# Kernel tuning notes

Hardware: AMD Instinct MI355X
Metric: run time of the kernel (lower is better)

The kernel has to match this reference:

```python
import jax, jax.numpy as jnp
import numpy as np


def setup_inputs() -> dict:
    key = jax.random.key(0)
    k_x, k_idx, k_sgn = jax.random.split(key, 3)
    batch, original_dim, proj_dim, c = 32, 1000000, 4096, 8
    x = jax.random.normal(k_x, (batch, original_dim), dtype=jnp.float32)
    rand_indices = jax.random.randint(k_idx, (original_dim, c), 0, proj_dim, dtype=jnp.int32)
    # random signs in {-1, +1}, matching torch.randint(0,2)*2-1 cast to int8
    rand_signs = (jax.random.randint(k_sgn, (original_dim, c), 0, 2, dtype=jnp.int32) * 2 - 1)
    return {"x": x, "rand_indices": rand_indices, "rand_signs": rand_signs,
            "proj_dim": proj_dim, "c": c}


def reference(x, rand_indices, rand_signs, proj_dim, c):
    # SJLT: each input coordinate d is scattered to c random output buckets
    # with random sign; normalized by 1/sqrt(c) so the sketch preserves norms.
    scale = jnp.asarray(1.0 / np.sqrt(c), dtype=x.dtype)
    batch = x.shape[0]
    out = jnp.zeros((batch, proj_dim), dtype=x.dtype)
    # c is a small fixed constant; loop over it, vectorize over batch & features.
    for j in range(c):
        vals = x * rand_signs[:, j].astype(x.dtype)      # [B, D]
        out = out.at[:, rand_indices[:, j]].add(vals)     # scatter-add along proj dim
    return out * scale
```

## Files before the change

### kernel.cpp

```cpp
#include <hip/hip_runtime.h>
#include <hip/hip_fp16.h>


#define D_TOTAL 1000000
#define PROJ    4096
#define C_SK    8
#define NE      (D_TOTAL * C_SK)
#define SCALE   0.35355339059327373f

#define NSEG    16
#define SEG_D   62500
#define CAPA2   8448
#define BINCAP_A 96
#define CAPH    96
#define TILE    4096
#define NBLK_A  ((NE + TILE - 1) / TILE)
#define NBLK_T  ((D_TOTAL + 255) / 256)
#define NSLICE  (NSEG * 2)

#define SMEM_FUSED 25088

#define CURA_OFF   0
#define XT_OFF     16384
#define XT_SZ      ((size_t)D_TOTAL * 32 * 2)
#define LISTA_OFF  (XT_OFF + XT_SZ)
#define LISTA_SZ   ((size_t)NSEG * 64 * CAPA2 * 4)
#define PART_OFF   (LISTA_OFF + LISTA_SZ)
#define PART_SZ    ((size_t)NSLICE * PROJ * 32 * 4)
#define WS_NEED    (PART_OFF + PART_SZ)

__global__ void init_cursors_kernel(int* __restrict__ curA) {
    int i = blockIdx.x * blockDim.x + threadIdx.x;
    if (i < NSEG * 64) curA[i] = i * CAPA2;
}

template<int BC>
__device__ __forceinline__ void rank_and_stage(bool ok, int kb, int payload,
                                               int* __restrict__ cnt,
                                               int* __restrict__ stage,
                                               int* __restrict__ gcur,
                                               int* __restrict__ glist,
                                               int gcur_idx, int glim) {
    if (ok) {
        const int pos = atomicAdd(&cnt[kb], 1);
        if (pos < BC) {
            stage[kb * BC + pos] = payload;
        } else {
            const int gp = atomicAdd(&gcur[gcur_idx], 1);
            if (gp < glim) glist[gp] = payload;
        }
    }
}

template<int BC>
__device__ __forceinline__ void flush_bins(int* __restrict__ cnt,
                                           int* __restrict__ basek,
                                           const int* __restrict__ stage,
                                           int* __restrict__ gcur,
                                           int* __restrict__ glist,
                                           int gidx0, int capPer) {
    const int tid = threadIdx.x;
    if (tid < 64) {
        const int m = min(cnt[tid], BC);
        cnt[tid]   = m;
        basek[tid] = atomicAdd(&gcur[gidx0 + tid], m);
    }
    __syncthreads();
    const int w = tid >> 6, lane = tid & 63;
    #pragma unroll 1
    for (int bi = 0; bi < 16; ++bi) {
        const int kb  = w * 16 + bi;
        const int m   = cnt[kb];
        const int gb  = basek[kb];
        const int lim = (gidx0 + kb + 1) * capPer;
        for (int i = lane; i < m; i += 64)
            if (gb + i < lim) glist[gb + i] = stage[kb * BC + i];
    }
}

__device__ __forceinline__ void pass_a_body(int abid, char* smem,
                                            const int* __restrict__ idx,
                                            const int* __restrict__ sgn,
                                            int* __restrict__ curA,
                                            int* __restrict__ listA) {
    int* stage = (int*)smem;
    int* cnt   = (int*)(smem + 64 * BINCAP_A * 4);
    int* basek = cnt + 64;
    const int tid = threadIdx.x;
    if (tid < 64) cnt[tid] = 0;
    __syncthreads();

    const int d_lo = abid * 512;
    const int seg  = d_lo / SEG_D;
    const bool boundary = ((d_lo + 511) / SEG_D) != seg;
    const int v0 = abid * (TILE / 4);

    #pragma unroll 1
    for (int k = 0; k < TILE / 1024; ++k) {
        const int vi = v0 + k * 256 + tid;
        const bool okv = vi < NE / 4;
        int4 i4 = {0,0,0,0}, s4 = {0,0,0,0};
        if (okv) { i4 = ((const int4*)idx)[vi]; s4 = ((const int4*)sgn)[vi]; }
        const int g0 = vi * 4;
        #pragma unroll
        for (int m = 0; m < 4; ++m) {
            const int bucket = (m == 0) ? i4.x : (m == 1) ? i4.y : (m == 2) ? i4.z : i4.w;
            const int sg     = (m == 0) ? s4.x : (m == 1) ? s4.y : (m == 2) ? s4.z : s4.w;
            const int kb = okv ? (bucket >> 6) : 0;
            const int payload = (g0 + m) | ((bucket & 63) << 24)
                              | (int)((unsigned)sg & 0x80000000u);
            if (!boundary) {
                rank_and_stage<BINCAP_A>(okv, kb, payload, cnt, stage, curA, listA,
                                         seg * 64 + kb, (seg * 64 + kb + 1) * CAPA2);
            } else if (okv) {
                const int segE = ((g0 + m) >> 3) / SEG_D;
                const int bin  = segE * 64 + kb;
                const int gp = atomicAdd(&curA[bin], 1);
                if (gp < (bin + 1) * CAPA2) listA[gp] = payload;
            }
        }
    }
    __syncthreads();
    flush_bins<BINCAP_A>(cnt, basek, stage, curA, listA, seg * 64, CAPA2);
}

__device__ __forceinline__ void transpose_body(int tbid, char* smem,
                                               const float* __restrict__ x,
                                               unsigned short* __restrict__ xT) {
    unsigned short (*tile)[260] = (unsigned short(*)[260])smem;
    const int tid = threadIdx.x;
    const int d0  = tbid * 256;
    const int row = tid >> 3;
    const int c8  = tid & 7;

    if (d0 + 256 <= D_TOTAL) {
        #pragma unroll
        for (int k = 0; k < 8; ++k) {
            const int c = (c8 + 8 * k) * 4;
            const float4 v = *(const float4*)(x + (size_t)row * D_TOTAL + d0 + c);
            unsigned short h[4];
            h[0] = __half_as_ushort(__float2half(v.x));
            h[1] = __half_as_ushort(__float2half(v.y));
            h[2] = __half_as_ushort(__float2half(v.z));
            h[3] = __half_as_ushort(__float2half(v.w));
            *(uint2*)&tile[row][c] = *(const uint2*)h;
        }
    } else {
        for (int k = 0; k < 8; ++k) {
            const int c = (c8 + 8 * k) * 4;
            for (int m = 0; m < 4; ++m) {
                const int d = d0 + c + m;
                tile[row][c + m] = __half_as_ushort(
                    __float2half((d < D_TOTAL) ? x[(size_t)row * D_TOTAL + d] : 0.f));
            }
        }
    }
    __syncthreads();

    const int part = tid & 3;
    #pragma unroll
    for (int k = 0; k < 4; ++k) {
        const int dl = k * 64 + (tid >> 2);
        if (d0 + dl < D_TOTAL) {
            unsigned short h[8];
            #pragma unroll
            for (int i = 0; i < 8; ++i)
                h[i] = tile[part * 8 + i][dl];
            *(uint4*)(xT + ((size_t)(d0 + dl)) * 32 + part * 8) = *(const uint4*)h;
        }
    }
}

__global__ __launch_bounds__(256, 6)
void pass_a_transpose_kernel(const int* __restrict__ idx, const int* __restrict__ sgn,
                             int* __restrict__ curA, int* __restrict__ listA,
                             const float* __restrict__ x, unsigned short* __restrict__ xT) {
    __shared__ char smem[SMEM_FUSED];
    const int id = blockIdx.x;
    if ((id % 3 == 0) && (id / 3 < NBLK_A)) {
        pass_a_body(id / 3, smem, idx, sgn, curA, listA);
    } else {
        const int tbid = id - id / 3 - ((id % 3) ? 1 : 0);
        if (tbid < NBLK_T) transpose_body(tbid, smem, x, xT);
    }
}

__global__ __launch_bounds__(256, 6)
void gather_part_kernel(const int* __restrict__ curA, const int* __restrict__ listA,
                        const unsigned short* __restrict__ xT,
                        float* __restrict__ partial, float* __restrict__ out) {
    __shared__ int stage[64 * CAPH];
    __shared__ int cnt[64];
    const int tid = threadIdx.x;
    const int gid = blockIdx.x;
    const int seg  = (gid & 7) + 8 * (gid >> 10);
    const int rest = (gid >> 3) & 127;
    const int kbA  = rest >> 1;
    const int half = rest & 1;
    const int part = seg * 64 + kbA;

    if (tid < 64) cnt[tid] = 0;
    __syncthreads();

    const int pstart = part * CAPA2;
    const int pcount = min(curA[part] - pstart, CAPA2);
    const int hn = (pcount + 1) >> 1;
    const int t0 = half * hn;
    const int t1 = min(t0 + hn, pcount);

    for (int i = t0 + tid; i < t1; i += 256) {
        const int e  = listA[pstart + i];
        const int kb = (e >> 24) & 63;
        const int pos = atomicAdd(&cnt[kb], 1);
        if (pos < CAPH) {
            stage[kb * CAPH + pos] = e;
        } else {
            int d = (e & 0x7FFFFF) >> 3;
            d = min(d, D_TOTAL - 1);
            const float s = (e < 0) ? -SCALE : SCALE;
            const int p = kbA * 64 + kb;
            for (int b = 0; b < 32; ++b) {
                const float v = __half2float(*(const __half*)(xT + (size_t)d * 32 + b));
                unsafeAtomicAdd(out + (size_t)b * PROJ + p, s * v);
            }
        }
    }
    __syncthreads();

    const int w    = tid >> 6;
    const int lane = tid & 63;
    const int slot = lane >> 2;
    const int bq   = lane & 3;
    #pragma unroll 1
    for (int bi = 0; bi < 16; ++bi) {
        const int kb = w * 16 + bi;
        const int n  = min(cnt[kb], CAPH);
        float a0=0.f,a1=0.f,a2=0.f,a3=0.f,a4=0.f,a5=0.f,a6=0.f,a7=0.f;
        #pragma unroll 2
        for (int base = 0; base < n; base += 16) {
            const int  e  = base + slot;
            const bool ok = e < n;
            const int  pl = stage[kb * CAPH + (ok ? e : 0)];
            int d = (pl & 0x7FFFFF) >> 3;
            d = min(d, D_TOTAL - 1);
            const float s = ok ? ((pl < 0) ? -1.f : 1.f) : 0.f;
            const uint4 hv = *(const uint4*)(xT + (size_t)d * 32 + bq * 8);
            float2 f;
            f = __half22float2(*(const __half2*)&hv.x); a0 = fmaf(s, f.x, a0); a1 = fmaf(s, f.y, a1);
            f = __half22float2(*(const __half2*)&hv.y); a2 = fmaf(s, f.x, a2); a3 = fmaf(s, f.y, a3);
            f = __half22float2(*(const __half2*)&hv.z); a4 = fmaf(s, f.x, a4); a5 = fmaf(s, f.y, a5);
            f = __half22float2(*(const __half2*)&hv.w); a6 = fmaf(s, f.x, a6); a7 = fmaf(s, f.y, a7);
        }
        #pragma unroll
        for (int m = 4; m <= 32; m <<= 1) {
            a0 += __shfl_xor(a0, m, 64); a1 += __shfl_xor(a1, m, 64);
            a2 += __shfl_xor(a2, m, 64); a3 += __shfl_xor(a3, m, 64);
            a4 += __shfl_xor(a4, m, 64); a5 += __shfl_xor(a5, m, 64);
            a6 += __shfl_xor(a6, m, 64); a7 += __shfl_xor(a7, m, 64);
        }
        if (lane < 4) {
            float v[8] = {a0,a1,a2,a3,a4,a5,a6,a7};
            const size_t slice = (size_t)(seg * 2 + half);
            float* dst = partial + (slice * PROJ + (size_t)(kbA * 64 + kb)) * 32 + lane * 8;
            #pragma unroll
            for (int i = 0; i < 8; ++i) dst[i] = v[i];
        }
    }
}

__global__ __launch_bounds__(256)
void reduce_kernel(const float* __restrict__ partial, float* __restrict__ out) {
    const int gtid = blockIdx.x * 256 + threadIdx.x;
    const int p = gtid & (PROJ - 1);
    const int b = gtid >> 12;
    float s = 0.f;
    #pragma unroll
    for (int sg = 0; sg < NSLICE; ++sg)
        s += partial[((size_t)(sg * PROJ + p)) * 32 + b];
    const size_t o = (size_t)b * PROJ + p;
    out[o] = out[o] + s * SCALE;
}

#define BG 8
#define NCHUNK 64
#define BLOCK 1024
__global__ __launch_bounds__(BLOCK, 4)
void sjlt_scatter_fallback(const float* __restrict__ x,
                           const int* __restrict__ idx,
                           const int* __restrict__ sgn,
                           float* __restrict__ out) {
    __shared__ float acc[BG * PROJ];
    const int tid = threadIdx.x;
    #pragma unroll
    for (int i = 0; i < (BG * PROJ) / BLOCK; ++i) acc[i * BLOCK + tid] = 0.0f;
    __syncthreads();
    const int chunk = D_TOTAL / NCHUNK;
    const int d0 = blockIdx.x * chunk;
    const int d1 = d0 + chunk;
    const int bg = blockIdx.y * BG;
    for (int d = d0 + tid; d < d1; d += BLOCK) {
        const int4 i0 = *(const int4*)(idx + (size_t)d * C_SK);
        const int4 i1 = *(const int4*)(idx + (size_t)d * C_SK + 4);
        const int4 s0 = *(const int4*)(sgn + (size_t)d * C_SK);
        const int4 s1 = *(const int4*)(sgn + (size_t)d * C_SK + 4);
        #pragma unroll
        for (int b = 0; b < BG; ++b) {
            const float xv = __builtin_nontemporal_load(x + (size_t)(bg + b) * D_TOTAL + d);
            const unsigned xb = __float_as_uint(xv);
            float* accb = acc + b * PROJ;
            atomicAdd(accb + i0.x, __uint_as_float(xb ^ ((unsigned)s0.x & 0x80000000u)));
            atomicAdd(accb + i0.y, __uint_as_float(xb ^ ((unsigned)s0.y & 0x80000000u)));
            atomicAdd(accb + i0.z, __uint_as_float(xb ^ ((unsigned)s0.z & 0x80000000u)));
            atomicAdd(accb + i0.w, __uint_as_float(xb ^ ((unsigned)s0.w & 0x80000000u)));
            atomicAdd(accb + i1.x, __uint_as_float(xb ^ ((unsigned)s1.x & 0x80000000u)));
            atomicAdd(accb + i1.y, __uint_as_float(xb ^ ((unsigned)s1.y & 0x80000000u)));
            atomicAdd(accb + i1.z, __uint_as_float(xb ^ ((unsigned)s1.z & 0x80000000u)));
            atomicAdd(accb + i1.w, __uint_as_float(xb ^ ((unsigned)s1.w & 0x80000000u)));
        }
    }
    __syncthreads();
    #pragma unroll
    for (int i = 0; i < (BG * PROJ) / BLOCK; ++i) {
        const int lin = i * BLOCK + tid;
        const int b = lin >> 12;
        const int pp = lin & (PROJ - 1);
        unsafeAtomicAdd(out + (size_t)(bg + b) * PROJ + pp, acc[lin] * SCALE);
    }
}

extern "C" void kernel_launch(void* const* d_in, const int* in_sizes, int n_in,
                              void* d_out, int out_size, void* d_ws, size_t ws_size,
                              hipStream_t stream) {
    const float* x   = (const float*)d_in[0];
    const int*   idx = (const int*)d_in[1];
    const int*   sgn = (const int*)d_in[2];
    float*       out = (float*)d_out;

    if (ws_size < WS_NEED) {
        (void)hipMemsetAsync(out, 0, (size_t)out_size * sizeof(float), stream);
        dim3 grid(NCHUNK, 32 / BG);
        sjlt_scatter_fallback<<<grid, BLOCK, 0, stream>>>(x, idx, sgn, out);
        return;
    }

    char* ws = (char*)d_ws;
    int*            curA    = (int*)(ws + CURA_OFF);
    unsigned short* xT      = (unsigned short*)(ws + XT_OFF);
    int*            listA   = (int*)(ws + LISTA_OFF);
    float*          partial = (float*)(ws + PART_OFF);

    (void)hipMemsetAsync(out, 0, (size_t)out_size * sizeof(float), stream);
    init_cursors_kernel<<<4, 256, 0, stream>>>(curA);
    pass_a_transpose_kernel<<<NBLK_A + NBLK_T, 256, 0, stream>>>(
        idx, sgn, curA, listA, x, xT);
    gather_part_kernel<<<2048, 256, 0, stream>>>(curA, listA, xT, partial, out);
    reduce_kernel<<<(32 * PROJ) / 256, 256, 0, stream>>>(partial, out);
}
```

Baseline: 370.4 us.

## Replace bucket-sort gather pipeline with LDS atomic scatter plus partial reduction

Drops the multi-pass bucket-sort pipeline (cursor init, index binning, fp16 transpose of x, gather, reduce). In its place, each 1024-thread block owns a chunk of D and 8 batch rows and scatter-adds signed x values into a 128KB LDS accumulator with atomics. Each block then writes its partial tile to workspace, and a second kernel sums the 64 chunk partials with vector loads and scales the result. This removes the fp16 transpose, the intermediate lists and the memset, but idx/sgn are now re-read once per batch group (4x) and the kernel depends on LDS atomic throughput with only one block per CU, so occupancy is low.

```diff
diff --git a/kernel.cpp b/kernel.cpp
--- a/kernel.cpp
+++ b/kernel.cpp
@@ -1,288 +1,97 @@
 #include <hip/hip_runtime.h>
-#include <hip/hip_fp16.h>
 
 
 #define D_TOTAL 1000000
 #define PROJ    4096
 #define C_SK    8
-#define NE      (D_TOTAL * C_SK)
 #define SCALE   0.35355339059327373f
 
-#define NSEG    16
-#define SEG_D   62500
-#define CAPA2   8448
-#define BINCAP_A 96
-#define CAPH    96
-#define TILE    4096
-#define NBLK_A  ((NE + TILE - 1) / TILE)
-#define NBLK_T  ((D_TOTAL + 255) / 256)
-#define NSLICE  (NSEG * 2)
+#define NCHUNK  64
+#define CHUNK_D (D_TOTAL / NCHUNK)
+#define NBG     4
+#define SBLK    1024
 
-#define SMEM_FUSED 25088
+typedef int          ni4 __attribute__((ext_vector_type(4)));
+typedef float        nf4 __attribute__((ext_vector_type(4)));
 
-#define CURA_OFF   0
-#define XT_OFF     16384
-#define XT_SZ      ((size_t)D_TOTAL * 32 * 2)
-#define LISTA_OFF  (XT_OFF + XT_SZ)
-#define LISTA_SZ   ((size_t)NSEG * 64 * CAPA2 * 4)
-#define PART_OFF   (LISTA_OFF + LISTA_SZ)
-#define PART_SZ    ((size_t)NSLICE * PROJ * 32 * 4)
-#define WS_NEED    (PART_OFF + PART_SZ)
+#define PART_SZ    ((size_t)NBG * NCHUNK * 8 * PROJ * 4)
+#define WS_NEED    PART_SZ
 
-__global__ void init_cursors_kernel(int* __restrict__ curA) {
-    int i = blockIdx.x * blockDim.x + threadIdx.x;
-    if (i < NSEG * 64) curA[i] = i * CAPA2;
-}
+__global__ __launch_bounds__(1024)
+void scatter_kernel(const float* __restrict__ x, const int* __restrict__ idx,
+                    const int* __restrict__ sgn, float* __restrict__ partial) {
+    __shared__ float acc[8 * PROJ];
+    const int tid   = threadIdx.x;
+    const int gid   = blockIdx.x;
+    const int bg    = gid >> 6;
+    const int chunk = gid & 63;
+    const int d0    = chunk * CHUNK_D;
 
-template<int BC>
-__device__ __forceinline__ void rank_and_stage(bool ok, int kb, int payload,
-                                               int* __restrict__ cnt,
-                                               int* __restrict__ stage,
-                                               int* __restrict__ gcur,
-                                               int* __restrict__ glist,
-                                               int gcur_idx, int glim) {
-    if (ok) {
-        const int pos = atomicAdd(&cnt[kb], 1);
-        if (pos < BC) {
-            stage[kb * BC + pos] = payload;
-        } else {
-            const int gp = atomicAdd(&gcur[gcur_idx], 1);
-            if (gp < glim) glist[gp] = payload;
-        }
-    }
-}
-
-template<int BC>
-__device__ __forceinline__ void flush_bins(int* __restrict__ cnt,
-                                           int* __restrict__ basek,
-                                           const int* __restrict__ stage,
-                                           int* __restrict__ gcur,
-                                           int* __restrict__ glist,
-                                           int gidx0, int capPer) {
-    const int tid = threadIdx.x;
-    if (tid < 64) {
-        const int m = min(cnt[tid], BC);
-        cnt[tid]   = m;
-        basek[tid] = atomicAdd(&gcur[gidx0 + tid], m);
-    }
-    __syncthreads();
-    const int w = tid >> 6, lane = tid & 63;
-    #pragma unroll 1
-    for (int bi = 0; bi < 16; ++bi) {
-        const int kb  = w * 16 + bi;
-        const int m   = cnt[kb];
-        const int gb  = basek[kb];
-        const int lim = (gidx0 + kb + 1) * capPer;
-        for (int i = lane; i < m; i += 64)
-            if (gb + i < lim) glist[gb + i] = stage[kb * BC + i];
-    }
-}
-
-__device__ __forceinline__ void pass_a_body(int abid, char* smem,
-                                            const int* __restrict__ idx,
-                                            const int* __restrict__ sgn,
-                                            int* __restrict__ curA,
-                                            int* __restrict__ listA) {
-    int* stage = (int*)smem;
-    int* cnt   = (int*)(smem + 64 * BINCAP_A * 4);
-    int* basek = cnt + 64;
-    const int tid = threadIdx.x;
-    if (tid < 64) cnt[tid] = 0;
+    #pragma unroll
+    for (int i = 0; i < 8; ++i)
+        ((nf4*)acc)[tid + i * SBLK] = (nf4){0.f, 0.f, 0.f, 0.f};
     __syncthreads();
 
-    const int d_lo = abid * 512;
-    const int seg  = d_lo / SEG_D;
-    const bool boundary = ((d_lo + 511) / SEG_D) != seg;
-    const int v0 = abid * (TILE / 4);
+    const float* xb = x + (size_t)(bg * 8) * D_TOTAL;
 
     #pragma unroll 1
-    for (int k = 0; k < TILE / 1024; ++k) {
-        const int vi = v0 + k * 256 + tid;
-        const bool okv = vi < NE / 4;
-        int4 i4 = {0,0,0,0}, s4 = {0,0,0,0};
-        if (okv) { i4 = ((const int4*)idx)[vi]; s4 = ((const int4*)sgn)[vi]; }
-        const int g0 = vi * 4;
-        #pragma unroll
-        for (int m = 0; m < 4; ++m) {
-            const int bucket = (m == 0) ? i4.x : (m == 1) ? i4.y : (m == 2) ? i4.z : i4.w;
-            const int sg     = (m == 0) ? s4.x : (m == 1) ? s4.y : (m == 2) ? s4.z : s4.w;
-            const int kb = okv ? (bucket >> 6) : 0;
-            const int payload = (g0 + m) | ((bucket & 63) << 24)
-                              | (int)((unsigned)sg & 0x80000000u);
-            if (!boundary) {
-                rank_and_stage<BINCAP_A>(okv, kb, payload, cnt, stage, curA, listA,
-                                         seg * 64 + kb, (seg * 64 + kb + 1) * CAPA2);
-            } else if (okv) {
-                const int segE = ((g0 + m) >> 3) / SEG_D;
-                const int bin  = segE * 64 + kb;
-                const int gp = atomicAdd(&curA[bin], 1);
-                if (gp < (bin + 1) * CAPA2) listA[gp] = payload;
-            }
-        }
-    }
-    __syncthreads();
-    flush_bins<BINCAP_A>(cnt, basek, stage, curA, listA, seg * 64, CAPA2);
-}
-
-__device__ __forceinline__ void transpose_body(int tbid, char* smem,
-                                               const float* __restrict__ x,
-                                               unsigned short* __restrict__ xT) {
-    unsigned short (*tile)[260] = (unsigned short(*)[260])smem;
-    const int tid = threadIdx.x;
-    const int d0  = tbid * 256;
-    const int row = tid >> 3;
-    const int c8  = tid & 7;
-
-    if (d0 + 256 <= D_TOTAL) {
-        #pragma unroll
-        for (int k = 0; k < 8; ++k) {
-            const int c = (c8 + 8 * k) * 4;
-            const float4 v = *(const float4*)(x + (size_t)row * D_TOTAL + d0 + c);
-            unsigned short h[4];
-            h[0] = __half_as_ushort(__float2half(v.x));
-            h[1] = __half_as_ushort(__float2half(v.y));
-            h[2] = __half_as_ushort(__float2half(v.z));
-            h[3] = __half_as_ushort(__float2half(v.w));
-            *(uint2*)&tile[row][c] = *(const uint2*)h;
-        }
-    } else {
-        for (int k = 0; k < 8; ++k) {
-            const int c = (c8 + 8 * k) * 4;
-            for (int m = 0; m < 4; ++m) {
-                const int d = d0 + c + m;
-                tile[row][c + m] = __half_as_ushort(
-                    __float2half((d < D_TOTAL) ? x[(size_t)row * D_TOTAL + d] : 0.f));
+    for (int k = 0; k < (CHUNK_D + SBLK - 1) / SBLK; ++k) {
+        const int dd = k * SBLK + tid;
+        if (dd < CHUNK_D) {
+            const int d = d0 + dd;
+            const ni4 i0 = *(const ni4*)(idx + (size_t)d * C_SK);
+            const ni4 i1 = *(const ni4*)(idx + (size_t)d * C_SK + 4);
+            const ni4 s0 = *(const ni4*)(sgn + (size_t)d * C_SK);
+            const ni4 s1 = *(const ni4*)(sgn + (size_t)d * C_SK + 4);
+            unsigned xv[8];
+            #pragma unroll
+            for (int b = 0; b < 8; ++b)
+                xv[b] = __builtin_nontemporal_load(
+                    (const unsigned*)(xb + (size_t)b * D_TOTAL) + d);
+            #pragma unroll
+            for (int j = 0; j < 8; ++j) {
+                const int      p  = (j < 4) ? i0[j] : i1[j - 4];
+                const unsigned sb = ((unsigned)((j < 4) ? s0[j] : s1[j - 4]))
+                                    & 0x80000000u;
+                float* a = acc + p;
+                #pragma unroll
+                for (int b = 0; b < 8; ++b)
+                    atomicAdd(a + b * PROJ, __uint_as_float(xv[b] ^ sb));
             }
         }
     }
     __syncthreads();
 
-    const int part = tid & 3;
+    float* dst = partial + (size_t)gid * (8 * PROJ);
     #pragma unroll
-    for (int k = 0; k < 4; ++k) {
-        const int dl = k * 64 + (tid >> 2);
-        if (d0 + dl < D_TOTAL) {
-            unsigned short h[8];
-            #pragma unroll
-            for (int i = 0; i < 8; ++i)
-                h[i] = tile[part * 8 + i][dl];
-            *(uint4*)(xT + ((size_t)(d0 + dl)) * 32 + part * 8) = *(const uint4*)h;
-        }
-    }
-}
-
-__global__ __launch_bounds__(256, 6)
-void pass_a_transpose_kernel(const int* __restrict__ idx, const int* __restrict__ sgn,
-                             int* __restrict__ curA, int* __restrict__ listA,
-                             const float* __restrict__ x, unsigned short* __restrict__ xT) {
-    __shared__ char smem[SMEM_FUSED];
-    const int id = blockIdx.x;
-    if ((id % 3 == 0) && (id / 3 < NBLK_A)) {
-        pass_a_body(id / 3, smem, idx, sgn, curA, listA);
-    } else {
-        const int tbid = id - id / 3 - ((id % 3) ? 1 : 0);
-        if (tbid < NBLK_T) transpose_body(tbid, smem, x, xT);
-    }
-}
-
-__global__ __launch_bounds__(256, 6)
-void gather_part_kernel(const int* __restrict__ curA, const int* __restrict__ listA,
-                        const unsigned short* __restrict__ xT,
-                        float* __restrict__ partial, float* __restrict__ out) {
-    __shared__ int stage[64 * CAPH];
-    __shared__ int cnt[64];
-    const int tid = threadIdx.x;
-    const int gid = blockIdx.x;
-    const int seg  = (gid & 7) + 8 * (gid >> 10);
-    const int rest = (gid >> 3) & 127;
-    const int kbA  = rest >> 1;
-    const int half = rest & 1;
-    const int part = seg * 64 + kbA;
-
-    if (tid < 64) cnt[tid] = 0;
-    __syncthreads();
-
-    const int pstart = part * CAPA2;
-    const int pcount = min(curA[part] - pstart, CAPA2);
-    const int hn = (pcount + 1) >> 1;
-    const int t0 = half * hn;
-    const int t1 = min(t0 + hn, pcount);
-
-    for (int i = t0 + tid; i < t1; i += 256) {
-        const int e  = listA[pstart + i];
-        const int kb = (e >> 24) & 63;
-        const int pos = atomicAdd(&cnt[kb], 1);
-        if (pos < CAPH) {
-            stage[kb * CAPH + pos] = e;
-        } else {
-            int d = (e & 0x7FFFFF) >> 3;
-            d = min(d, D_TOTAL - 1);
-            const float s = (e < 0) ? -SCALE : SCALE;
-            const int p = kbA * 64 + kb;
-            for (int b = 0; b < 32; ++b) {
-                const float v = __half2float(*(const __half*)(xT + (size_t)d * 32 + b));
-                unsafeAtomicAdd(out + (size_t)b * PROJ + p, s * v);
-            }
-        }
-    }
-    __syncthreads();
-
-    const int w    = tid >> 6;
-    const int lane = tid & 63;
-    const int slot = lane >> 2;
-    const int bq   = lane & 3;
-    #pragma unroll 1
-    for (int bi = 0; bi < 16; ++bi) {
-        const int kb = w * 16 + bi;
-        const int n  = min(cnt[kb], CAPH);
-        float a0=0.f,a1=0.f,a2=0.f,a3=0.f,a4=0.f,a5=0.f,a6=0.f,a7=0.f;
-        #pragma unroll 2
-        for (int base = 0; base < n; base += 16) {
-            const int  e  = base + slot;
-            const bool ok = e < n;
-            const int  pl = stage[kb * CAPH + (ok ? e : 0)];
-            int d = (pl & 0x7FFFFF) >> 3;
-            d = min(d, D_TOTAL - 1);
-            const float s = ok ? ((pl < 0) ? -1.f : 1.f) : 0.f;
-            const uint4 hv = *(const uint4*)(xT + (size_t)d * 32 + bq * 8);
-            float2 f;
-            f = __half22float2(*(const __half2*)&hv.x); a0 = fmaf(s, f.x, a0); a1 = fmaf(s, f.y, a1);
-            f = __half22float2(*(const __half2*)&hv.y); a2 = fmaf(s, f.x, a2); a3 = fmaf(s, f.y, a3);
-            f = __half22float2(*(const __half2*)&hv.z); a4 = fmaf(s, f.x, a4); a5 = fmaf(s, f.y, a5);
-            f = __half22float2(*(const __half2*)&hv.w); a6 = fmaf(s, f.x, a6); a7 = fmaf(s, f.y, a7);
-        }
-        #pragma unroll
-        for (int m = 4; m <= 32; m <<= 1) {
-            a0 += __shfl_xor(a0, m, 64); a1 += __shfl_xor(a1, m, 64);
-            a2 += __shfl_xor(a2, m, 64); a3 += __shfl_xor(a3, m, 64);
-            a4 += __shfl_xor(a4, m, 64); a5 += __shfl_xor(a5, m, 64);
-            a6 += __shfl_xor(a6, m, 64); a7 += __shfl_xor(a7, m, 64);
-        }
-        if (lane < 4) {
-            float v[8] = {a0,a1,a2,a3,a4,a5,a6,a7};
-            const size_t slice = (size_t)(seg * 2 + half);
-            float* dst = partial + (slice * PROJ + (size_t)(kbA * 64 + kb)) * 32 + lane * 8;
-            #pragma unroll
-            for (int i = 0; i < 8; ++i) dst[i] = v[i];
-        }
+    for (int i = 0; i < 8; ++i) {
+        const int o = tid + i * SBLK;
+        __builtin_nontemporal_store(((const nf4*)acc)[o], (nf4*)dst + o);
     }
 }
 
 __global__ __launch_bounds__(256)
-void reduce_kernel(const float* __restrict__ partial, float* __restrict__ out) {
-    const int gtid = blockIdx.x * 256 + threadIdx.x;
-    const int p = gtid & (PROJ - 1);
-    const int b = gtid >> 12;
-    float s = 0.f;
-    #pragma unroll
-    for (int sg = 0; sg < NSLICE; ++sg)
-        s += partial[((size_t)(sg * PROJ + p)) * 32 + b];
-    const size_t o = (size_t)b * PROJ + p;
-    out[o] = out[o] + s * SCALE;
+void reduce_scatter_kernel(const float* __restrict__ partial,
+                           float* __restrict__ out) {
+    const int t  = blockIdx.x * 256 + threadIdx.x;
+    const int p4 = t & 1023;
+    const int b  = t >> 10;
+    const int bg = b >> 3, lb = b & 7;
+    const float* base = partial + (size_t)bg * 64 * (8 * PROJ)
+                      + (size_t)lb * PROJ + (size_t)p4 * 4;
+    nf4 s = {0.f, 0.f, 0.f, 0.f};
+    #pragma unroll 4
+    for (int c = 0; c < NCHUNK; ++c) {
+        const nf4 v = __builtin_nontemporal_load(
+            (const nf4*)(base + (size_t)c * (8 * PROJ)));
+        s[0] += v[0]; s[1] += v[1]; s[2] += v[2]; s[3] += v[3];
+    }
+    s[0] *= SCALE; s[1] *= SCALE; s[2] *= SCALE; s[3] *= SCALE;
+    *(nf4*)(out + (size_t)b * PROJ + (size_t)p4 * 4) = s;
 }
 
 #define BG 8
-#define NCHUNK 64
+#define FCHUNK 64
 #define BLOCK 1024
 __global__ __launch_bounds__(BLOCK, 4)
 void sjlt_scatter_fallback(const float* __restrict__ x,
@@ -294,7 +103,7 @@
     #pragma unroll
     for (int i = 0; i < (BG * PROJ) / BLOCK; ++i) acc[i * BLOCK + tid] = 0.0f;
     __syncthreads();
-    const int chunk = D_TOTAL / NCHUNK;
+    const int chunk = D_TOTAL / FCHUNK;
     const int d0 = blockIdx.x * chunk;
     const int d1 = d0 + chunk;
     const int bg = blockIdx.y * BG;
@@ -338,21 +147,12 @@
 
     if (ws_size < WS_NEED) {
         (void)hipMemsetAsync(out, 0, (size_t)out_size * sizeof(float), stream);
-        dim3 grid(NCHUNK, 32 / BG);
+        dim3 grid(FCHUNK, 32 / BG);
         sjlt_scatter_fallback<<<grid, BLOCK, 0, stream>>>(x, idx, sgn, out);
         return;
     }
 
-    char* ws = (char*)d_ws;
-    int*            curA    = (int*)(ws + CURA_OFF);
-    unsigned short* xT      = (unsigned short*)(ws + XT_OFF);
-    int*            listA   = (int*)(ws + LISTA_OFF);
-    float*          partial = (float*)(ws + PART_OFF);
-
-    (void)hipMemsetAsync(out, 0, (size_t)out_size * sizeof(float), stream);
-    init_cursors_kernel<<<4, 256, 0, stream>>>(curA);
-    pass_a_transpose_kernel<<<NBLK_A + NBLK_T, 256, 0, stream>>>(
-        idx, sgn, curA, listA, x, xT);
-    gather_part_kernel<<<2048, 256, 0, stream>>>(curA, listA, xT, partial, out);
-    reduce_kernel<<<(32 * PROJ) / 256, 256, 0, stream>>>(partial, out);
+    float* partial = (float*)d_ws;
+    scatter_kernel<<<NBG * NCHUNK, SBLK, 0, stream>>>(x, idx, sgn, partial);
+    reduce_scatter_kernel<<<(32 * PROJ / 4) / 256, 256, 0, stream>>>(partial, out);
 }
```

Result: slower. 1.459 ms (+293.8%).
